# Performance work log

Measured on AMD Instinct MI355X. Metric: run time of the kernel, lower is better.

Reference implementation:

```python
import jax, jax.numpy as jnp
import numpy as np

COMMITMENT_COST = 0.25
NUM_EMBEDDINGS = 1024
EMBEDDING_DIM = 64


def setup_inputs() -> dict:
    key = jax.random.key(0)
    k1, k2 = jax.random.split(key)
    z = jax.random.normal(k1, (32, EMBEDDING_DIM, 64, 64), dtype=jnp.float32)
    # nn.Embedding init: uniform(-1/K, 1/K)
    lim = 1.0 / NUM_EMBEDDINGS
    embeddings = jax.random.uniform(k2, (NUM_EMBEDDINGS, EMBEDDING_DIM),
                                    dtype=jnp.float32, minval=-lim, maxval=lim)
    return {"z": z, "embeddings": embeddings}


def reference(z, embeddings):
    # z: [B, C, H, W] with C == embedding_dim
    B, C, H, W = z.shape
    z_perm = jnp.transpose(z, (0, 2, 3, 1))          # [B, H, W, C]
    flat_z = z_perm.reshape(-1, C)                    # [N, C]

    # squared L2 distances: ||z||^2 - 2 z.E^T + ||E||^2  -> [N, K]
    distances = (jnp.sum(flat_z * flat_z, axis=1, keepdims=True)
                 - 2.0 * flat_z @ embeddings.T
                 + jnp.sum(embeddings * embeddings, axis=1))
    encoding_indices = jnp.argmin(distances, axis=1)  # [N]

    # direct gather (equivalent to one-hot @ embeddings)
    quantized = embeddings[encoding_indices].reshape(z_perm.shape)  # [B,H,W,C]

    commitment_loss = COMMITMENT_COST * jnp.mean(
        (jax.lax.stop_gradient(quantized) - z_perm) ** 2)
    codebook_loss = jnp.mean((quantized - jax.lax.stop_gradient(z_perm)) ** 2)
    loss = commitment_loss + codebook_loss

    # straight-through estimator
    quantized_st = z_perm + jax.lax.stop_gradient(quantized - z_perm)
    out = jnp.transpose(quantized_st, (0, 3, 1, 2))   # [B, C, H, W]
    return out, loss
```

## Files before the change

### kernel.cpp

```cpp
#include <hip/hip_runtime.h>
#include <hip/hip_bf16.h>

#define CDIM   64
#define HWDIM  4096
#define NCODES 1024
#define NELEM  8388608
#define NBLOCK 1024
#define NPART  (NBLOCK * 8)
#define LDSSZ  (65536 + 16 * 68 * 4)

typedef float f32x4 __attribute__((ext_vector_type(4)));
typedef long  longx2 __attribute__((ext_vector_type(2)));

__device__ __forceinline__ unsigned asu(float f) {
    union { float f; unsigned u; } v; v.f = f; return v.u;
}
__device__ __forceinline__ float asf(unsigned u) {
    union { unsigned u; float f; } v; v.u = u; return v.f;
}
__device__ __forceinline__ void gload_lds16(const void* g, void* l) {
    __builtin_amdgcn_global_load_lds(
        (const __attribute__((address_space(1))) void*)g,
        (__attribute__((address_space(3))) void*)l, 16, 0, 0);
}

__global__ void vq_prep(const float* __restrict__ E,
                        unsigned char* __restrict__ Eb,
                        float* __restrict__ biasS) {
    int t = blockIdx.x * blockDim.x + threadIdx.x;
    if (t < NCODES) {
        const float4* ev = (const float4*)(E + t * CDIM);
        float s = 0.f;
        #pragma unroll
        for (int g = 0; g < 4; ++g) {
            float4 va = ev[2 * g], vb = ev[2 * g + 1];
            float4 vc = ev[8 + 2 * g], vd = ev[9 + 2 * g];
            s = fmaf(va.x, va.x, s); s = fmaf(va.y, va.y, s);
            s = fmaf(va.z, va.z, s); s = fmaf(va.w, va.w, s);
            s = fmaf(vb.x, vb.x, s); s = fmaf(vb.y, vb.y, s);
            s = fmaf(vb.z, vb.z, s); s = fmaf(vb.w, vb.w, s);
            s = fmaf(vc.x, vc.x, s); s = fmaf(vc.y, vc.y, s);
            s = fmaf(vc.z, vc.z, s); s = fmaf(vc.w, vc.w, s);
            s = fmaf(vd.x, vd.x, s); s = fmaf(vd.y, vd.y, s);
            s = fmaf(vd.z, vd.z, s); s = fmaf(vd.w, vd.w, s);
            const float S = 16384.f;
            int i0 = __builtin_amdgcn_cvt_pk_fp8_f32(va.x * S, va.y * S, 0, false);
            i0     = __builtin_amdgcn_cvt_pk_fp8_f32(va.z * S, va.w * S, i0, true);
            int i1 = __builtin_amdgcn_cvt_pk_fp8_f32(vb.x * S, vb.y * S, 0, false);
            i1     = __builtin_amdgcn_cvt_pk_fp8_f32(vb.z * S, vb.w * S, i1, true);
            int i2 = __builtin_amdgcn_cvt_pk_fp8_f32(vc.x * S, vc.y * S, 0, false);
            i2     = __builtin_amdgcn_cvt_pk_fp8_f32(vc.z * S, vc.w * S, i2, true);
            int i3 = __builtin_amdgcn_cvt_pk_fp8_f32(vd.x * S, vd.y * S, 0, false);
            i3     = __builtin_amdgcn_cvt_pk_fp8_f32(vd.z * S, vd.w * S, i3, true);
            const int slot = g ^ ((t >> 1) & 3);
            int4 q; q.x = i0; q.y = i1; q.z = i2; q.w = i3;
            *(int4*)(Eb + t * CDIM + slot * 16) = q;
        }
        biasS[t] = -8192.f * s;
    }
}

__global__ __launch_bounds__(512)
void vq_main(const float* __restrict__ z,
             const float* __restrict__ E,
             const unsigned char* __restrict__ Eb,
             const float* __restrict__ biasS,
             float* __restrict__ out,
             float* __restrict__ partial) {
    extern __shared__ char smem[];
    unsigned char* sEb = (unsigned char*)smem;
    float (*sBiasT)[68] = (float(*)[68])(smem + 65536);

    const int lane = threadIdx.x & 63;
    const int wave = threadIdx.x >> 6;
    const int lrow = lane & 15;
    const int lgrp = lane >> 4;

    const int n0 = blockIdx.x * 128 + wave * 16;
    const int b  = n0 >> 12;
    const int hw = n0 & 4095;
    const float* zb   = z   + (size_t)b * (CDIM * HWDIM);
    float*       outb = out + (size_t)b * (CDIM * HWDIM);

    #pragma unroll
    for (int i = 0; i < 8; ++i) {
        const int cid = i * 512 + (int)threadIdx.x;
        gload_lds16(Eb + cid * 16, sEb + cid * 16);
    }
    {
        const int i = (int)threadIdx.x;
        sBiasT[i & 15][i >> 4] = biasS[i];
        const int i2 = i + 512;
        sBiasT[i2 & 15][i2 >> 4] = biasS[i2];
    }

    float szz = 0.f;
    long a0, a1;
    {
        float zv[8];
        #pragma unroll
        for (int j = 0; j < 8; ++j) {
            float v = zb[(8 * lgrp + j) * HWDIM + hw + lrow];
            szz = fmaf(v, v, szz); zv[j] = v;
        }
        int dlo = __builtin_amdgcn_cvt_pk_fp8_f32(zv[0], zv[1], 0, false);
        dlo     = __builtin_amdgcn_cvt_pk_fp8_f32(zv[2], zv[3], dlo, true);
        int dhi = __builtin_amdgcn_cvt_pk_fp8_f32(zv[4], zv[5], 0, false);
        dhi     = __builtin_amdgcn_cvt_pk_fp8_f32(zv[6], zv[7], dhi, true);
        a0 = (long)(unsigned)dlo | ((long)dhi << 32);
        #pragma unroll
        for (int j = 0; j < 8; ++j) {
            float v = zb[(32 + 8 * lgrp + j) * HWDIM + hw + lrow];
            szz = fmaf(v, v, szz); zv[j] = v;
        }
        dlo = __builtin_amdgcn_cvt_pk_fp8_f32(zv[0], zv[1], 0, false);
        dlo = __builtin_amdgcn_cvt_pk_fp8_f32(zv[2], zv[3], dlo, true);
        dhi = __builtin_amdgcn_cvt_pk_fp8_f32(zv[4], zv[5], 0, false);
        dhi = __builtin_amdgcn_cvt_pk_fp8_f32(zv[6], zv[7], dhi, true);
        a1 = (long)(unsigned)dlo | ((long)dhi << 32);
    }

    float run[4] = {-3.0e38f, -3.0e38f, -3.0e38f, -3.0e38f};

    __syncthreads();

    const char* pa = (const char*)sEb + lrow * CDIM
                   + ((lgrp ^ ((lrow >> 1) & 3)) << 4);
    const float* pbias = &sBiasT[lrow][0];
    unsigned codev = (unsigned)lrow;

    for (int ch = 0; ch < 8; ++ch) {
        f32x4 bq0 = *(const f32x4*)(pbias);
        f32x4 bq1 = *(const f32x4*)(pbias + 4);
        #pragma unroll
        for (int j = 0; j < 8; ++j) {
            longx2 bb = *(const longx2*)(pa + j * 1024);
            const float bv = (j < 4) ? bq0[j] : bq1[j - 4];
            f32x4 ci = {bv, bv, bv, bv};
            f32x4 acc = __builtin_amdgcn_mfma_f32_16x16x32_fp8_fp8(a0, bb.x, ci, 0, 0, 0);
            acc = __builtin_amdgcn_mfma_f32_16x16x32_fp8_fp8(a1, bb.y, acc, 0, 0, 0);
            const unsigned code = codev + (unsigned)(j * 16);
            #pragma unroll
            for (int r = 0; r < 4; ++r)
                run[r] = fmaxf(run[r], asf((asu(acc[r]) & 0xFFFFFC00u) | code));
        }
        pa += 8192; pbias += 8; codev += 128;
    }

    #pragma unroll
    for (int m = 1; m <= 8; m <<= 1)
        #pragma unroll
        for (int r = 0; r < 4; ++r)
            run[r] = fmaxf(run[r], __shfl_xor(run[r], m, 64));

    int idxe;
    {
        const int src = (lrow >> 2) << 4;
        float g0 = __shfl(run[0], src, 64);
        float g1 = __shfl(run[1], src, 64);
        float g2 = __shfl(run[2], src, 64);
        float g3 = __shfl(run[3], src, 64);
        float sel = (lrow & 2) ? ((lrow & 1) ? g3 : g2)
                               : ((lrow & 1) ? g1 : g0);
        idxe = (int)(asu(sel) & 1023u);
    }

    {
        const f32x4* ep  = (const f32x4*)(E + idxe * CDIM      + 8 * lgrp);
        const f32x4* ep2 = (const f32x4*)(E + idxe * CDIM + 32 + 8 * lgrp);
        f32x4 qa = ep[0], qb = ep[1], qc = ep2[0], qd = ep2[1];
        float* ob = outb + hw + lrow;
        #pragma unroll
        for (int j = 0; j < 4; ++j) {
            ob[(8 * lgrp + j)          * HWDIM] = qa[j];
            ob[(8 * lgrp + 4 + j)      * HWDIM] = qb[j];
            ob[(32 + 8 * lgrp + j)     * HWDIM] = qc[j];
            ob[(32 + 8 * lgrp + 4 + j) * HWDIM] = qd[j];
        }
    }

    float dsum = run[0] + run[1] + run[2] + run[3];
    float contrib = szz + ((lrow == 0) ? (-1.220703125e-4f * dsum) : 0.f);
    #pragma unroll
    for (int m = 32; m >= 1; m >>= 1) contrib += __shfl_xor(contrib, m, 64);
    if (lane == 0) partial[blockIdx.x * 8 + wave] = contrib;
}

__global__ __launch_bounds__(1024)
void vq_fin(const float* __restrict__ partial,
            float* __restrict__ out) {
    __shared__ float red[16];
    const int tid = threadIdx.x;
    float s = 0.f;
    #pragma unroll
    for (int i = 0; i < NPART / 1024; ++i) s += partial[i * 1024 + tid];
    #pragma unroll
    for (int m = 32; m >= 1; m >>= 1) s += __shfl_xor(s, m, 64);
    if ((tid & 63) == 0) red[tid >> 6] = s;
    __syncthreads();
    if (tid == 0) {
        float tot = 0.f;
        #pragma unroll
        for (int w = 0; w < 16; ++w) tot += red[w];
        out[NELEM] = 1.25f * tot / (float)NELEM;
    }
}

extern "C" void kernel_launch(void* const* d_in, const int* in_sizes, int n_in,
                              void* d_out, int out_size, void* d_ws, size_t ws_size,
                              hipStream_t stream) {
    const float* z = (const float*)d_in[0];
    const float* E = (const float*)d_in[1];
    float* out = (float*)d_out;

    unsigned char* Eb = (unsigned char*)d_ws;
    float* biasS      = (float*)((char*)d_ws + 65536);
    float* partial    = (float*)((char*)d_ws + 65536 + 4096);

    hipFuncSetAttribute((const void*)vq_main,
                        hipFuncAttributeMaxDynamicSharedMemorySize, LDSSZ);

    vq_prep<<<4, 256, 0, stream>>>(E, Eb, biasS);
    vq_main<<<NBLOCK, 512, LDSSZ, stream>>>(z, E, Eb, biasS, out, partial);
    vq_fin<<<1, 1024, 0, stream>>>(partial, out);
}
```

Measured before the change: 34.51 us.

## Process two 16-row tiles per wave to reuse codebook LDS loads

Each wave now handles 32 vectors instead of 16, reusing every codebook fragment loaded from LDS for two MFMA chains, and the grid is halved to 512 blocks. This halves the LDS codebook reads and block-level codebook staging per vector and gives more independent MFMAs to hide latency. In exchange it raises register pressure and leaves fewer blocks to spread across the compute units, which may reduce occupancy and load balance.

```diff
diff --git a/kernel.cpp b/kernel.cpp
--- a/kernel.cpp
+++ b/kernel.cpp
@@ -5,7 +5,7 @@
 #define HWDIM  4096
 #define NCODES 1024
 #define NELEM  8388608
-#define NBLOCK 1024
+#define NBLOCK 512
 #define NPART  (NBLOCK * 8)
 #define LDSSZ  (65536 + 16 * 68 * 4)
 
@@ -76,7 +76,7 @@
     const int lrow = lane & 15;
     const int lgrp = lane >> 4;
 
-    const int n0 = blockIdx.x * 128 + wave * 16;
+    const int n0 = blockIdx.x * 256 + wave * 32;
     const int b  = n0 >> 12;
     const int hw = n0 & 4095;
     const float* zb   = z   + (size_t)b * (CDIM * HWDIM);
@@ -95,32 +95,41 @@
     }
 
     float szz = 0.f;
-    long a0, a1;
+    long a00, a01, a10, a11;
     {
         float zv[8];
         #pragma unroll
-        for (int j = 0; j < 8; ++j) {
-            float v = zb[(8 * lgrp + j) * HWDIM + hw + lrow];
-            szz = fmaf(v, v, szz); zv[j] = v;
-        }
-        int dlo = __builtin_amdgcn_cvt_pk_fp8_f32(zv[0], zv[1], 0, false);
-        dlo     = __builtin_amdgcn_cvt_pk_fp8_f32(zv[2], zv[3], dlo, true);
-        int dhi = __builtin_amdgcn_cvt_pk_fp8_f32(zv[4], zv[5], 0, false);
-        dhi     = __builtin_amdgcn_cvt_pk_fp8_f32(zv[6], zv[7], dhi, true);
-        a0 = (long)(unsigned)dlo | ((long)dhi << 32);
-        #pragma unroll
-        for (int j = 0; j < 8; ++j) {
-            float v = zb[(32 + 8 * lgrp + j) * HWDIM + hw + lrow];
-            szz = fmaf(v, v, szz); zv[j] = v;
-        }
-        dlo = __builtin_amdgcn_cvt_pk_fp8_f32(zv[0], zv[1], 0, false);
-        dlo = __builtin_amdgcn_cvt_pk_fp8_f32(zv[2], zv[3], dlo, true);
-        dhi = __builtin_amdgcn_cvt_pk_fp8_f32(zv[4], zv[5], 0, false);
-        dhi = __builtin_amdgcn_cvt_pk_fp8_f32(zv[6], zv[7], dhi, true);
-        a1 = (long)(unsigned)dlo | ((long)dhi << 32);
-    }
-
-    float run[4] = {-3.0e38f, -3.0e38f, -3.0e38f, -3.0e38f};
+        for (int t = 0; t < 2; ++t) {
+            #pragma unroll
+            for (int j = 0; j < 8; ++j) {
+                float v = zb[(8 * lgrp + j) * HWDIM + hw + t * 16 + lrow];
+                szz = fmaf(v, v, szz); zv[j] = v;
+            }
+            int dlo = __builtin_amdgcn_cvt_pk_fp8_f32(zv[0], zv[1], 0, false);
+            dlo     = __builtin_amdgcn_cvt_pk_fp8_f32(zv[2], zv[3], dlo, true);
+            int dhi = __builtin_amdgcn_cvt_pk_fp8_f32(zv[4], zv[5], 0, false);
+            dhi     = __builtin_amdgcn_cvt_pk_fp8_f32(zv[6], zv[7], dhi, true);
+            long lo = (long)(unsigned)dlo | ((long)dhi << 32);
+            #pragma unroll
+            for (int j = 0; j < 8; ++j) {
+                float v = zb[(32 + 8 * lgrp + j) * HWDIM + hw + t * 16 + lrow];
+                szz = fmaf(v, v, szz); zv[j] = v;
+            }
+            dlo = __builtin_amdgcn_cvt_pk_fp8_f32(zv[0], zv[1], 0, false);
+            dlo = __builtin_amdgcn_cvt_pk_fp8_f32(zv[2], zv[3], dlo, true);
+            dhi = __builtin_amdgcn_cvt_pk_fp8_f32(zv[4], zv[5], 0, false);
+            dhi = __builtin_amdgcn_cvt_pk_fp8_f32(zv[6], zv[7], dhi, true);
+            long hi = (long)(unsigned)dlo | ((long)dhi << 32);
+            if (t == 0) { a00 = lo; a01 = hi; }
+            else        { a10 = lo; a11 = hi; }
+        }
+    }
+
+    float run[2][4];
+    #pragma unroll
+    for (int t = 0; t < 2; ++t)
+        #pragma unroll
+        for (int r = 0; r < 4; ++r) run[t][r] = -3.0e38f;
 
     __syncthreads();
 
@@ -137,39 +146,48 @@
             longx2 bb = *(const longx2*)(pa + j * 1024);
             const float bv = (j < 4) ? bq0[j] : bq1[j - 4];
             f32x4 ci = {bv, bv, bv, bv};
-            f32x4 acc = __builtin_amdgcn_mfma_f32_16x16x32_fp8_fp8(a0, bb.x, ci, 0, 0, 0);
-            acc = __builtin_amdgcn_mfma_f32_16x16x32_fp8_fp8(a1, bb.y, acc, 0, 0, 0);
+            f32x4 ac0 = __builtin_amdgcn_mfma_f32_16x16x32_fp8_fp8(a00, bb.x, ci, 0, 0, 0);
+            ac0 = __builtin_amdgcn_mfma_f32_16x16x32_fp8_fp8(a01, bb.y, ac0, 0, 0, 0);
+            f32x4 ac1 = __builtin_amdgcn_mfma_f32_16x16x32_fp8_fp8(a10, bb.x, ci, 0, 0, 0);
+            ac1 = __builtin_amdgcn_mfma_f32_16x16x32_fp8_fp8(a11, bb.y, ac1, 0, 0, 0);
             const unsigned code = codev + (unsigned)(j * 16);
             #pragma unroll
+            for (int r = 0; r < 4; ++r) {
+                run[0][r] = fmaxf(run[0][r], asf((asu(ac0[r]) & 0xFFFFFC00u) | code));
+                run[1][r] = fmaxf(run[1][r], asf((asu(ac1[r]) & 0xFFFFFC00u) | code));
+            }
+        }
+        pa += 8192; pbias += 8; codev += 128;
+    }
+
+    #pragma unroll
+    for (int m = 1; m <= 8; m <<= 1)
+        #pragma unroll
+        for (int t = 0; t < 2; ++t)
+            #pragma unroll
             for (int r = 0; r < 4; ++r)
-                run[r] = fmaxf(run[r], asf((asu(acc[r]) & 0xFFFFFC00u) | code));
-        }
-        pa += 8192; pbias += 8; codev += 128;
-    }
-
-    #pragma unroll
-    for (int m = 1; m <= 8; m <<= 1)
-        #pragma unroll
-        for (int r = 0; r < 4; ++r)
-            run[r] = fmaxf(run[r], __shfl_xor(run[r], m, 64));
-
-    int idxe;
-    {
+                run[t][r] = fmaxf(run[t][r], __shfl_xor(run[t][r], m, 64));
+
+    int idxe[2];
+    #pragma unroll
+    for (int t = 0; t < 2; ++t) {
         const int src = (lrow >> 2) << 4;
-        float g0 = __shfl(run[0], src, 64);
-        float g1 = __shfl(run[1], src, 64);
-        float g2 = __shfl(run[2], src, 64);
-        float g3 = __shfl(run[3], src, 64);
+        float g0 = __shfl(run[t][0], src, 64);
+        float g1 = __shfl(run[t][1], src, 64);
+        float g2 = __shfl(run[t][2], src, 64);
+        float g3 = __shfl(run[t][3], src, 64);
         float sel = (lrow & 2) ? ((lrow & 1) ? g3 : g2)
                                : ((lrow & 1) ? g1 : g0);
-        idxe = (int)(asu(sel) & 1023u);
-    }
-
-    {
-        const f32x4* ep  = (const f32x4*)(E + idxe * CDIM      + 8 * lgrp);
-        const f32x4* ep2 = (const f32x4*)(E + idxe * CDIM + 32 + 8 * lgrp);
+        idxe[t] = (int)(asu(sel) & 1023u);
+    }
+
+    #pragma unroll
+    for (int t = 0; t < 2; ++t) {
+        const int idxr = idxe[t];
+        const f32x4* ep  = (const f32x4*)(E + idxr * CDIM      + 8 * lgrp);
+        const f32x4* ep2 = (const f32x4*)(E + idxr * CDIM + 32 + 8 * lgrp);
         f32x4 qa = ep[0], qb = ep[1], qc = ep2[0], qd = ep2[1];
-        float* ob = outb + hw + lrow;
+        float* ob = outb + hw + t * 16 + lrow;
         #pragma unroll
         for (int j = 0; j < 4; ++j) {
             ob[(8 * lgrp + j)          * HWDIM] = qa[j];
@@ -179,7 +197,11 @@
         }
     }
 
-    float dsum = run[0] + run[1] + run[2] + run[3];
+    float dsum = 0.f;
+    #pragma unroll
+    for (int t = 0; t < 2; ++t)
+        #pragma unroll
+        for (int r = 0; r < 4; ++r) dsum += run[t][r];
     float contrib = szz + ((lrow == 0) ? (-1.220703125e-4f * dsum) : 0.f);
     #pragma unroll
     for (int m = 32; m >= 1; m >>= 1) contrib += __shfl_xor(contrib, m, 64);
```

Result: faster. 32.99 us (median of 3 runs) (-4.4%).
